# Kernel tuning notes

Hardware: AMD Instinct MI355X
Metric: run time of the kernel (lower is better)

## Reference

```python
import jax, jax.numpy as jnp
import numpy as np

NUM_HEADS = 12


def setup_inputs() -> dict:
    key = jax.random.key(0)
    k1, k2, k3 = jax.random.split(key, 3)
    B, N, C = 4, 2048, 768
    x = jax.random.normal(k1, (B, N, C), dtype=jnp.float32)
    # Linear weights stored as [in, out] so y = x @ W (+ b); matches torch Linear math.
    w_qkv = jax.random.normal(k2, (C, 3 * C), dtype=jnp.float32) * (C ** -0.5)
    w_proj = jax.random.normal(k3, (C, C), dtype=jnp.float32) * (C ** -0.5)
    b_proj = jnp.zeros((C,), dtype=jnp.float32)
    return {"x": x, "w_qkv": w_qkv, "w_proj": w_proj, "b_proj": b_proj}


def reference(x, w_qkv, w_proj, b_proj):
    B, N, C = x.shape
    H = NUM_HEADS
    D = C // H
    scale = D ** -0.5
    qkv = (x @ w_qkv).reshape(B, N, 3, H, D)
    qkv = jnp.transpose(qkv, (2, 0, 3, 1, 4))  # [3, B, H, N, D]
    q, k, v = qkv[0], qkv[1], qkv[2]
    attn = jnp.einsum("bhnd,bhmd->bhnm", q, k) * scale  # [B, H, N, N]
    # causal mask (triu with offset 1), filled with -finfo.max as in the torch code
    causal_mask = jnp.triu(jnp.ones((N, N), dtype=bool), k=1)
    mask_value = -jnp.finfo(attn.dtype).max
    attn = jnp.where(causal_mask, mask_value, attn)
    attn = jax.nn.softmax(attn, axis=-1)
    attn = jnp.nan_to_num(attn)
    out = jnp.einsum("bhnm,bhmd->bhnd", attn, v)  # [B, H, N, D]
    out = jnp.transpose(out, (0, 2, 1, 3)).reshape(B, N, C)
    return out @ w_proj + b_proj
```

## Files before the change

kernel.cpp:

```cpp
#include <hip/hip_runtime.h>
#include <hip/hip_bf16.h>
#include <math.h>

#define BATCH 4
#define SEQ   2048
#define CDIM  768
#define NHEAD 12
#define HDIM  64
#define MROWS (BATCH*SEQ)
#define QKVC  (3*CDIM)

typedef __bf16    bf16x8 __attribute__((ext_vector_type(8)));
typedef _Float16  f16x8  __attribute__((ext_vector_type(8)));
typedef _Float16  f16x4  __attribute__((ext_vector_type(4)));
typedef float     f32x4  __attribute__((ext_vector_type(4)));

__device__ __forceinline__ void async16(const void* g, void* l) {
  __builtin_amdgcn_global_load_lds(
      (const __attribute__((address_space(1))) void*)g,
      (__attribute__((address_space(3))) void*)l, 16, 0, 0);
}

__global__ __launch_bounds__(256) void cast_f32_bf16(
    const float* __restrict__ in, __bf16* __restrict__ out, int n8) {
  int i = blockIdx.x * 256 + threadIdx.x;
  if (i >= n8) return;
  float4 a = reinterpret_cast<const float4*>(in)[i * 2];
  float4 b = reinterpret_cast<const float4*>(in)[i * 2 + 1];
  bf16x8 o;
  o[0] = (__bf16)a.x; o[1] = (__bf16)a.y; o[2] = (__bf16)a.z; o[3] = (__bf16)a.w;
  o[4] = (__bf16)b.x; o[5] = (__bf16)b.y; o[6] = (__bf16)b.z; o[7] = (__bf16)b.w;
  reinterpret_cast<bf16x8*>(out)[i] = o;
}

__global__ __launch_bounds__(256) void transpose_cast(
    const float* __restrict__ w, __bf16* __restrict__ wt, int K, int N) {
  __shared__ float sh[32][33];
  const int n0 = blockIdx.x * 32, k0 = blockIdx.y * 32;
  const int tx = threadIdx.x, ty = threadIdx.y;
#pragma unroll
  for (int i = 0; i < 4; ++i)
    sh[ty + i * 8][tx] = w[(size_t)(k0 + ty + i * 8) * N + n0 + tx];
  __syncthreads();
#pragma unroll
  for (int i = 0; i < 4; ++i)
    wt[(size_t)(n0 + ty + i * 8) * K + k0 + tx] = (__bf16)sh[tx][ty + i * 8];
}

template <bool BF16OUT>
__global__ __launch_bounds__(256) void gemm_bf16_kernel(
    const __bf16* __restrict__ A, const __bf16* __restrict__ Bt,
    const float* __restrict__ bias, void* __restrict__ Cout,
    int M, int N, int K) {
  __shared__ __align__(16) __bf16 As[128 * 32];
  __shared__ __align__(16) __bf16 Bs[128 * 32];
  const int tid  = threadIdx.x;
  const int w    = tid >> 6;
  const int lane = tid & 63;
  const int quad = lane >> 4;
  const int lr   = lane & 15;
  const int wr   = w >> 1, wc = w & 1;
  const int mBase = blockIdx.y * 128, nBase = blockIdx.x * 128;

  f32x4 acc[4][4] = {};

  const int srow = lane >> 2;
  const int sk8  = (lane & 3) * 8;
  const __bf16* aSrc0 = A  + (size_t)(mBase + w * 32 + srow) * K + sk8;
  const __bf16* aSrc1 = aSrc0 + (size_t)16 * K;
  const __bf16* bSrc0 = Bt + (size_t)(nBase + w * 32 + srow) * K + sk8;
  const __bf16* bSrc1 = bSrc0 + (size_t)16 * K;
  __bf16* aDst0 = &As[(w * 32 + 0) * 32];
  __bf16* aDst1 = &As[(w * 32 + 16) * 32];
  __bf16* bDst0 = &Bs[(w * 32 + 0) * 32];
  __bf16* bDst1 = &Bs[(w * 32 + 16) * 32];

  for (int k0 = 0; k0 < K; k0 += 32) {
    __syncthreads();
    async16(aSrc0 + k0, aDst0);
    async16(aSrc1 + k0, aDst1);
    async16(bSrc0 + k0, bDst0);
    async16(bSrc1 + k0, bDst1);
    __syncthreads();

    bf16x8 af[4], bfr[4];
#pragma unroll
    for (int mt = 0; mt < 4; ++mt)
      af[mt] = *reinterpret_cast<const bf16x8*>(
          &As[(wr * 64 + mt * 16 + lr) * 32 + quad * 8]);
#pragma unroll
    for (int nt = 0; nt < 4; ++nt)
      bfr[nt] = *reinterpret_cast<const bf16x8*>(
          &Bs[(wc * 64 + nt * 16 + lr) * 32 + quad * 8]);
#pragma unroll
    for (int mt = 0; mt < 4; ++mt)
#pragma unroll
      for (int nt = 0; nt < 4; ++nt)
        acc[mt][nt] = __builtin_amdgcn_mfma_f32_16x16x32_bf16(
            af[mt], bfr[nt], acc[mt][nt], 0, 0, 0);
  }

#pragma unroll
  for (int mt = 0; mt < 4; ++mt) {
#pragma unroll
    for (int nt = 0; nt < 4; ++nt) {
      const int col = nBase + wc * 64 + nt * 16 + lr;
#pragma unroll
      for (int r = 0; r < 4; ++r) {
        const size_t row = (size_t)(mBase + wr * 64 + mt * 16 + quad * 4 + r);
        if (BF16OUT) {
          ((__bf16*)Cout)[row * N + col] = (__bf16)acc[mt][nt][r];
        } else {
          ((float*)Cout)[row * N + col] = acc[mt][nt][r] + bias[col];
        }
      }
    }
  }
}

__global__ __launch_bounds__(256) void swizzle_kv(
    const __bf16* __restrict__ qkv, __bf16* __restrict__ kF,
    _Float16* __restrict__ vF) {
  const int kt = blockIdx.x;
  const int hb = blockIdx.y;
  const int h = hb % NHEAD, b = hb / NHEAD;
  const int tid = threadIdx.x;

  __shared__ __align__(16) __bf16 Ksh[64][72];
  __shared__ __align__(16) _Float16 Vsh[64][72];

  const int sr = tid >> 3;
  const int sc = (tid & 7) * 8;
  const __bf16* kbase = qkv + (size_t)(b * SEQ + kt * 64) * QKVC + CDIM + h * HDIM;
  const __bf16* vbase = kbase + CDIM;

#pragma unroll
  for (int rr = 0; rr < 2; ++rr) {
    const int row = sr + rr * 32;
    bf16x8 kv = *reinterpret_cast<const bf16x8*>(kbase + (size_t)row * QKVC + sc);
    *reinterpret_cast<bf16x8*>(&Ksh[row][sc]) = kv;
    bf16x8 vv = *reinterpret_cast<const bf16x8*>(vbase + (size_t)row * QKVC + sc);
    f16x8 vf;
#pragma unroll
    for (int j = 0; j < 8; ++j) vf[j] = (_Float16)(float)vv[j];
    *reinterpret_cast<f16x8*>(&Vsh[row][sc]) = vf;
  }
  __syncthreads();

  const size_t tileOff = ((size_t)(hb * 32 + kt)) * 4096;

#pragma unroll
  for (int ss = 0; ss < 2; ++ss) {
    const int s = tid + ss * 256;
    const int f = s >> 6, lane = s & 63;
    const int nt = f >> 1, kc = f & 1;
    const int lq = lane >> 4, ll = lane & 15;
    bf16x8 frag = *reinterpret_cast<const bf16x8*>(
        &Ksh[nt * 16 + ll][kc * 32 + lq * 8]);
    *reinterpret_cast<bf16x8*>(&kF[tileOff + (size_t)f * 512 + lane * 8]) = frag;
  }
#pragma unroll
  for (int ss = 0; ss < 2; ++ss) {
    const int s = tid + ss * 256;
    const int g = s >> 6, lane = s & 63;
    const int nt = g >> 1, ph = g & 1;
    const int lq = lane >> 4, ll = lane & 15;
    f16x8 frag;
#pragma unroll
    for (int j = 0; j < 8; ++j)
      frag[j] = Vsh[nt * 16 + lq * 4 + (j & 3)][(ph * 2 + (j >> 2)) * 16 + ll];
    *reinterpret_cast<f16x8*>(&vF[tileOff + (size_t)g * 512 + lane * 8]) = frag;
  }
}

__global__ __launch_bounds__(256, 2) void flash_mfma_kernel(
    const __bf16* __restrict__ qkv, const __bf16* __restrict__ kF,
    const _Float16* __restrict__ vF, __bf16* __restrict__ out) {
  const int bid  = blockIdx.x;
  const int tid  = threadIdx.x;
  const int w    = tid >> 6;
  const int lane = tid & 63;
  const int quad = lane >> 4;
  const int lr   = lane & 15;

  const int x   = bid & 7;
  const int g   = bid >> 3;
  const int qt  = 31 - (g / 6);
  const int hb  = x * 6 + (g % 6);
  const int h   = hb % NHEAD, b = hb / NHEAD;

  __shared__ __align__(16) float Red[2][64 * 80];

  bf16x8 qf[4][2];
  {
    const float qs = 0.125f * 1.44269504088896f;
    const __bf16* qp = qkv + (size_t)(b * SEQ + qt * 64) * QKVC + h * HDIM;
#pragma unroll
    for (int qg = 0; qg < 4; ++qg)
#pragma unroll
      for (int kc = 0; kc < 2; ++kc) {
        bf16x8 qr = *reinterpret_cast<const bf16x8*>(
            qp + (size_t)(qg * 16 + lr) * QKVC + kc * 32 + quad * 8);
        bf16x8 f;
#pragma unroll
        for (int j = 0; j < 8; ++j) f[j] = (__bf16)((float)qr[j] * qs);
        qf[qg][kc] = f;
      }
  }

  f32x4 O[4][4] = {};
  f32x4 O4[4] = {};

  const __bf16*   kT = kF + ((size_t)(hb * 32)) * 4096 + lane * 8;
  const _Float16* vT = vF + ((size_t)(hb * 32)) * 4096 + lane * 8;
  const f16x4 vones = {(_Float16)1.f, (_Float16)1.f, (_Float16)1.f, (_Float16)1.f};

  for (int kt = w; kt <= qt; kt += 4) {
    bf16x8 kf[8];
    f16x8  vf8[8];
#pragma unroll
    for (int f = 0; f < 8; ++f)
      kf[f] = *reinterpret_cast<const bf16x8*>(kT + (size_t)kt * 4096 + f * 512);
#pragma unroll
    for (int gg = 0; gg < 8; ++gg)
      vf8[gg] = *reinterpret_cast<const f16x8*>(vT + (size_t)kt * 4096 + gg * 512);

#pragma unroll
    for (int nt = 0; nt < 4; ++nt) {
      f32x4 s[4];
#pragma unroll
      for (int qg = 0; qg < 4; ++qg) {
        f32x4 acc = (f32x4){0.f, 0.f, 0.f, 0.f};
        acc = __builtin_amdgcn_mfma_f32_16x16x32_bf16(kf[nt * 2 + 0], qf[qg][0], acc, 0, 0, 0);
        acc = __builtin_amdgcn_mfma_f32_16x16x32_bf16(kf[nt * 2 + 1], qf[qg][1], acc, 0, 0, 0);
        s[qg] = acc;
      }
      if (kt == qt) {
#pragma unroll
        for (int qg = 0; qg < 4; ++qg)
#pragma unroll
          for (int r = 0; r < 4; ++r)
            if (nt * 16 + quad * 4 + r > qg * 16 + lr) s[qg][r] = -1e30f;
      }
      f16x4 pa[4];
#pragma unroll
      for (int qg = 0; qg < 4; ++qg) {
        f16x4 t;
#pragma unroll
        for (int r = 0; r < 4; ++r)
          t[r] = (_Float16)__builtin_amdgcn_exp2f(s[qg][r]);
        pa[qg] = t;
      }
#pragma unroll
      for (int qg = 0; qg < 4; ++qg)
        O4[qg] = __builtin_amdgcn_mfma_f32_16x16x16f16(pa[qg], vones, O4[qg], 0, 0, 0);
#pragma unroll
      for (int dt = 0; dt < 4; ++dt) {
        const f16x8 vv = vf8[nt * 2 + (dt >> 1)];
        f16x4 vb;
#pragma unroll
        for (int j = 0; j < 4; ++j) vb[j] = vv[(dt & 1) * 4 + j];
#pragma unroll
        for (int qg = 0; qg < 4; ++qg)
          O[qg][dt] = __builtin_amdgcn_mfma_f32_16x16x16f16(pa[qg], vb, O[qg][dt], 0, 0, 0);
      }
    }
  }

  if (w == 1 || w == 3) {
    float* dst = Red[w >> 1];
#pragma unroll
    for (int qg = 0; qg < 4; ++qg)
#pragma unroll
      for (int dt = 0; dt < 4; ++dt)
        *reinterpret_cast<f32x4*>(&dst[((qg * 4 + dt) * 64 + lane) * 4]) = O[qg][dt];
#pragma unroll
    for (int qg = 0; qg < 4; ++qg)
      *reinterpret_cast<f32x4*>(&dst[((16 + qg) * 64 + lane) * 4]) = O4[qg];
  }
  __syncthreads();
  if (w == 0 || w == 2) {
    const float* src = Red[w >> 1];
#pragma unroll
    for (int qg = 0; qg < 4; ++qg)
#pragma unroll
      for (int dt = 0; dt < 4; ++dt)
        O[qg][dt] += *reinterpret_cast<const f32x4*>(&src[((qg * 4 + dt) * 64 + lane) * 4]);
#pragma unroll
    for (int qg = 0; qg < 4; ++qg)
      O4[qg] += *reinterpret_cast<const f32x4*>(&src[((16 + qg) * 64 + lane) * 4]);
  }
  __syncthreads();
  if (w == 2) {
    float* dst = Red[0];
#pragma unroll
    for (int qg = 0; qg < 4; ++qg)
#pragma unroll
      for (int dt = 0; dt < 4; ++dt)
        *reinterpret_cast<f32x4*>(&dst[((qg * 4 + dt) * 64 + lane) * 4]) = O[qg][dt];
#pragma unroll
    for (int qg = 0; qg < 4; ++qg)
      *reinterpret_cast<f32x4*>(&dst[((16 + qg) * 64 + lane) * 4]) = O4[qg];
  }
  __syncthreads();
  if (w == 0) {
    const float* src = Red[0];
#pragma unroll
    for (int qg = 0; qg < 4; ++qg)
#pragma unroll
      for (int dt = 0; dt < 4; ++dt)
        O[qg][dt] += *reinterpret_cast<const f32x4*>(&src[((qg * 4 + dt) * 64 + lane) * 4]);
#pragma unroll
    for (int qg = 0; qg < 4; ++qg)
      O4[qg] += *reinterpret_cast<const f32x4*>(&src[((16 + qg) * 64 + lane) * 4]);

    __bf16* obase = out + (size_t)(b * SEQ + qt * 64) * CDIM + h * HDIM;
#pragma unroll
    for (int qg = 0; qg < 4; ++qg) {
      float linv[4];
#pragma unroll
      for (int r = 0; r < 4; ++r) linv[r] = 1.f / O4[qg][r];
#pragma unroll
      for (int dt = 0; dt < 4; ++dt)
#pragma unroll
        for (int r = 0; r < 4; ++r)
          obase[(size_t)(qg * 16 + quad * 4 + r) * CDIM + dt * 16 + lr] =
              (__bf16)(O[qg][dt][r] * linv[r]);
    }
  }
}

extern "C" void kernel_launch(void* const* d_in, const int* in_sizes, int n_in,
                              void* d_out, int out_size, void* d_ws, size_t ws_size,
                              hipStream_t stream) {
  const float* x      = (const float*)d_in[0];
  const float* w_qkv  = (const float*)d_in[1];
  const float* w_proj = (const float*)d_in[2];
  const float* b_proj = (const float*)d_in[3];
  float* out = (float*)d_out;

  __bf16* qkv    = (__bf16*)d_ws;
  __bf16* attnb  = qkv + (size_t)MROWS * QKVC;
  __bf16* xb     = attnb + (size_t)MROWS * CDIM;
  __bf16* wqkvT  = xb + (size_t)MROWS * CDIM;
  __bf16* wprojT = wqkvT + (size_t)QKVC * CDIM;
  __bf16* kFb    = wprojT + (size_t)CDIM * CDIM;
  _Float16* vFb  = (_Float16*)(kFb + (size_t)48 * 32 * 4096);

  cast_f32_bf16<<<dim3((MROWS * CDIM / 8 + 255) / 256), dim3(256), 0, stream>>>(
      x, xb, MROWS * CDIM / 8);
  transpose_cast<<<dim3(QKVC / 32, CDIM / 32), dim3(32, 8), 0, stream>>>(
      w_qkv, wqkvT, CDIM, QKVC);
  transpose_cast<<<dim3(CDIM / 32, CDIM / 32), dim3(32, 8), 0, stream>>>(
      w_proj, wprojT, CDIM, CDIM);

  gemm_bf16_kernel<true><<<dim3(QKVC / 128, MROWS / 128), dim3(256), 0, stream>>>(
      xb, wqkvT, nullptr, qkv, MROWS, QKVC, CDIM);

  swizzle_kv<<<dim3(32, 48), dim3(256), 0, stream>>>(qkv, kFb, vFb);

  flash_mfma_kernel<<<dim3(1536), dim3(256), 0, stream>>>(qkv, kFb, vFb, attnb);

  gemm_bf16_kernel<false><<<dim3(CDIM / 128, MROWS / 128), dim3(256), 0, stream>>>(
      attnb, wprojT, b_proj, out, MROWS, CDIM, CDIM);
}
```

Measured before the change: 208.8 us.

## Fuse K/V fragment swizzle into QKV GEMM epilogue and deepen K step to 64

The QKV projection GEMM now writes K and V directly in the MFMA-fragment layouts the flash kernel consumes, so the separate swizzle_kv kernel and its extra read and write of K/V are removed. Both GEMMs also load two 32-wide K slices per barrier pair, which halves the number of synchronisation rounds and doubles the shared-memory tile. The cost is scattered, narrow stores in the K/V epilogue and higher LDS use per block, which may lower occupancy.

```diff
diff --git a/kernel.cpp b/kernel.cpp
--- a/kernel.cpp
+++ b/kernel.cpp
@@ -47,13 +47,14 @@
     wt[(size_t)(n0 + ty + i * 8) * K + k0 + tx] = (__bf16)sh[tx][ty + i * 8];
 }
 
-template <bool BF16OUT>
-__global__ __launch_bounds__(256) void gemm_bf16_kernel(
+template <int MODE>
+__global__ __launch_bounds__(256) void gemm_bk64_kernel(
     const __bf16* __restrict__ A, const __bf16* __restrict__ Bt,
     const float* __restrict__ bias, void* __restrict__ Cout,
+    __bf16* __restrict__ kF, _Float16* __restrict__ vF,
     int M, int N, int K) {
-  __shared__ __align__(16) __bf16 As[128 * 32];
-  __shared__ __align__(16) __bf16 Bs[128 * 32];
+  __shared__ __align__(16) __bf16 As[2][128 * 32];
+  __shared__ __align__(16) __bf16 Bs[2][128 * 32];
   const int tid  = threadIdx.x;
   const int w    = tid >> 6;
   const int lane = tid & 63;
@@ -70,106 +71,94 @@
   const __bf16* aSrc1 = aSrc0 + (size_t)16 * K;
   const __bf16* bSrc0 = Bt + (size_t)(nBase + w * 32 + srow) * K + sk8;
   const __bf16* bSrc1 = bSrc0 + (size_t)16 * K;
-  __bf16* aDst0 = &As[(w * 32 + 0) * 32];
-  __bf16* aDst1 = &As[(w * 32 + 16) * 32];
-  __bf16* bDst0 = &Bs[(w * 32 + 0) * 32];
-  __bf16* bDst1 = &Bs[(w * 32 + 16) * 32];
-
-  for (int k0 = 0; k0 < K; k0 += 32) {
+
+  for (int k0 = 0; k0 < K; k0 += 64) {
     __syncthreads();
-    async16(aSrc0 + k0, aDst0);
-    async16(aSrc1 + k0, aDst1);
-    async16(bSrc0 + k0, bDst0);
-    async16(bSrc1 + k0, bDst1);
+#pragma unroll
+    for (int kh = 0; kh < 2; ++kh) {
+      async16(aSrc0 + k0 + kh * 32, &As[kh][(w * 32 + 0) * 32]);
+      async16(aSrc1 + k0 + kh * 32, &As[kh][(w * 32 + 16) * 32]);
+      async16(bSrc0 + k0 + kh * 32, &Bs[kh][(w * 32 + 0) * 32]);
+      async16(bSrc1 + k0 + kh * 32, &Bs[kh][(w * 32 + 16) * 32]);
+    }
     __syncthreads();
 
-    bf16x8 af[4], bfr[4];
+#pragma unroll
+    for (int kh = 0; kh < 2; ++kh) {
+      bf16x8 af[4], bfr[4];
+#pragma unroll
+      for (int mt = 0; mt < 4; ++mt)
+        af[mt] = *reinterpret_cast<const bf16x8*>(
+            &As[kh][(wr * 64 + mt * 16 + lr) * 32 + quad * 8]);
+#pragma unroll
+      for (int nt = 0; nt < 4; ++nt)
+        bfr[nt] = *reinterpret_cast<const bf16x8*>(
+            &Bs[kh][(wc * 64 + nt * 16 + lr) * 32 + quad * 8]);
+#pragma unroll
+      for (int mt = 0; mt < 4; ++mt)
+#pragma unroll
+        for (int nt = 0; nt < 4; ++nt)
+          acc[mt][nt] = __builtin_amdgcn_mfma_f32_16x16x32_bf16(
+              af[mt], bfr[nt], acc[mt][nt], 0, 0, 0);
+    }
+  }
+
+  if (MODE == 1) {
 #pragma unroll
     for (int mt = 0; mt < 4; ++mt)
-      af[mt] = *reinterpret_cast<const bf16x8*>(
-          &As[(wr * 64 + mt * 16 + lr) * 32 + quad * 8]);
-#pragma unroll
-    for (int nt = 0; nt < 4; ++nt)
-      bfr[nt] = *reinterpret_cast<const bf16x8*>(
-          &Bs[(wc * 64 + nt * 16 + lr) * 32 + quad * 8]);
-#pragma unroll
-    for (int mt = 0; mt < 4; ++mt)
-#pragma unroll
-      for (int nt = 0; nt < 4; ++nt)
-        acc[mt][nt] = __builtin_amdgcn_mfma_f32_16x16x32_bf16(
-            af[mt], bfr[nt], acc[mt][nt], 0, 0, 0);
-  }
-
-#pragma unroll
-  for (int mt = 0; mt < 4; ++mt) {
-#pragma unroll
-    for (int nt = 0; nt < 4; ++nt) {
-      const int col = nBase + wc * 64 + nt * 16 + lr;
-#pragma unroll
-      for (int r = 0; r < 4; ++r) {
-        const size_t row = (size_t)(mBase + wr * 64 + mt * 16 + quad * 4 + r);
-        if (BF16OUT) {
-          ((__bf16*)Cout)[row * N + col] = (__bf16)acc[mt][nt][r];
-        } else {
+#pragma unroll
+      for (int nt = 0; nt < 4; ++nt) {
+        const int col = nBase + wc * 64 + nt * 16 + lr;
+#pragma unroll
+        for (int r = 0; r < 4; ++r) {
+          const size_t row = (size_t)(mBase + wr * 64 + mt * 16 + quad * 4 + r);
           ((float*)Cout)[row * N + col] = acc[mt][nt][r] + bias[col];
         }
       }
-    }
-  }
-}
-
-__global__ __launch_bounds__(256) void swizzle_kv(
-    const __bf16* __restrict__ qkv, __bf16* __restrict__ kF,
-    _Float16* __restrict__ vF) {
-  const int kt = blockIdx.x;
-  const int hb = blockIdx.y;
-  const int h = hb % NHEAD, b = hb / NHEAD;
-  const int tid = threadIdx.x;
-
-  __shared__ __align__(16) __bf16 Ksh[64][72];
-  __shared__ __align__(16) _Float16 Vsh[64][72];
-
-  const int sr = tid >> 3;
-  const int sc = (tid & 7) * 8;
-  const __bf16* kbase = qkv + (size_t)(b * SEQ + kt * 64) * QKVC + CDIM + h * HDIM;
-  const __bf16* vbase = kbase + CDIM;
-
-#pragma unroll
-  for (int rr = 0; rr < 2; ++rr) {
-    const int row = sr + rr * 32;
-    bf16x8 kv = *reinterpret_cast<const bf16x8*>(kbase + (size_t)row * QKVC + sc);
-    *reinterpret_cast<bf16x8*>(&Ksh[row][sc]) = kv;
-    bf16x8 vv = *reinterpret_cast<const bf16x8*>(vbase + (size_t)row * QKVC + sc);
-    f16x8 vf;
-#pragma unroll
-    for (int j = 0; j < 8; ++j) vf[j] = (_Float16)(float)vv[j];
-    *reinterpret_cast<f16x8*>(&Vsh[row][sc]) = vf;
-  }
-  __syncthreads();
-
-  const size_t tileOff = ((size_t)(hb * 32 + kt)) * 4096;
-
-#pragma unroll
-  for (int ss = 0; ss < 2; ++ss) {
-    const int s = tid + ss * 256;
-    const int f = s >> 6, lane = s & 63;
-    const int nt = f >> 1, kc = f & 1;
-    const int lq = lane >> 4, ll = lane & 15;
-    bf16x8 frag = *reinterpret_cast<const bf16x8*>(
-        &Ksh[nt * 16 + ll][kc * 32 + lq * 8]);
-    *reinterpret_cast<bf16x8*>(&kF[tileOff + (size_t)f * 512 + lane * 8]) = frag;
-  }
-#pragma unroll
-  for (int ss = 0; ss < 2; ++ss) {
-    const int s = tid + ss * 256;
-    const int g = s >> 6, lane = s & 63;
-    const int nt = g >> 1, ph = g & 1;
-    const int lq = lane >> 4, ll = lane & 15;
-    f16x8 frag;
-#pragma unroll
-    for (int j = 0; j < 8; ++j)
-      frag[j] = Vsh[nt * 16 + lq * 4 + (j & 3)][(ph * 2 + (j >> 2)) * 16 + ll];
-    *reinterpret_cast<f16x8*>(&vF[tileOff + (size_t)g * 512 + lane * 8]) = frag;
+  } else {
+    const int region = nBase / CDIM;
+    if (region == 0) {
+#pragma unroll
+      for (int mt = 0; mt < 4; ++mt)
+#pragma unroll
+        for (int nt = 0; nt < 4; ++nt) {
+          const int col = nBase + wc * 64 + nt * 16 + lr;
+#pragma unroll
+          for (int r = 0; r < 4; ++r) {
+            const size_t row = (size_t)(mBase + wr * 64 + mt * 16 + quad * 4 + r);
+            ((__bf16*)Cout)[row * N + col] = (__bf16)acc[mt][nt][r];
+          }
+        }
+    } else {
+      const int bb  = mBase >> 11;
+      const int ktB = ((mBase & 2047) >> 6) + wr;
+      const int hq  = ((nBase % CDIM) + wc * 64) >> 6;
+      const size_t tile = ((size_t)(bb * NHEAD + hq) * 32 + ktB) * 4096;
+      if (region == 1) {
+#pragma unroll
+        for (int mt = 0; mt < 4; ++mt)
+#pragma unroll
+          for (int nt = 0; nt < 4; ++nt) {
+            const size_t base = tile + (size_t)(mt * 2 + (nt >> 1)) * 512
+                + (((nt & 1) * 2 + (lr >> 3)) * 16) * 8 + (lr & 7);
+#pragma unroll
+            for (int r = 0; r < 4; ++r)
+              kF[base + (quad * 4 + r) * 8] = (__bf16)acc[mt][nt][r];
+          }
+      } else {
+#pragma unroll
+        for (int mt = 0; mt < 4; ++mt)
+#pragma unroll
+          for (int nt = 0; nt < 4; ++nt) {
+            f16x4 vp;
+#pragma unroll
+            for (int r = 0; r < 4; ++r) vp[r] = (_Float16)acc[mt][nt][r];
+            *reinterpret_cast<f16x4*>(
+                &vF[tile + (size_t)(mt * 2 + (nt >> 1)) * 512
+                    + (quad * 16 + lr) * 8 + (nt & 1) * 4]) = vp;
+          }
+      }
+    }
   }
 }
 
@@ -354,13 +343,11 @@
   transpose_cast<<<dim3(CDIM / 32, CDIM / 32), dim3(32, 8), 0, stream>>>(
       w_proj, wprojT, CDIM, CDIM);
 
-  gemm_bf16_kernel<true><<<dim3(QKVC / 128, MROWS / 128), dim3(256), 0, stream>>>(
-      xb, wqkvT, nullptr, qkv, MROWS, QKVC, CDIM);
-
-  swizzle_kv<<<dim3(32, 48), dim3(256), 0, stream>>>(qkv, kFb, vFb);
+  gemm_bk64_kernel<0><<<dim3(QKVC / 128, MROWS / 128), dim3(256), 0, stream>>>(
+      xb, wqkvT, nullptr, qkv, kFb, vFb, MROWS, QKVC, CDIM);
 
   flash_mfma_kernel<<<dim3(1536), dim3(256), 0, stream>>>(qkv, kFb, vFb, attnb);
 
-  gemm_bf16_kernel<false><<<dim3(CDIM / 128, MROWS / 128), dim3(256), 0, stream>>>(
-      attnb, wprojT, b_proj, out, MROWS, CDIM, CDIM);
-}
+  gemm_bk64_kernel<1><<<dim3(CDIM / 128, MROWS / 128), dim3(256), 0, stream>>>(
+      attnb, wprojT, b_proj, out, nullptr, nullptr, MROWS, CDIM, CDIM);
+}
```

Measured after the change: 195.3 us. -6.5%, faster.
